# Optimization experiments

Hardware: AMD Instinct MI355X
Metric: run time of the kernel (lower is better)

## Reference

```python
import jax, jax.numpy as jnp
import numpy as np

B, L, D, K = 64, 1024, 128, 256
SQRT_2D = float(np.sqrt(2 * D))


def _biamlp(x1, x2, Wi, bi, Wq, bq):
    # proj to 2*D, norm-weighted fusion, avg-pool(2)*2 (== pairwise sum), L2-normalize over dim 1
    f1 = x1 @ Wi + bi          # [B, L, 2D]
    f2 = x2 @ Wq + bq          # [B, L, 2D]
    n1 = jnp.linalg.norm(f1)   # global L2 norm (scalar), as torch.norm(., p=2)
    n2 = jnp.linalg.norm(f2)
    e = (n1 / (n1 + n2)) * f1 + (n2 / (n1 + n2)) * f2
    b, l, c = e.shape
    z = e.reshape(b, l, c // 2, 2).mean(-1) * 2.0   # AvgPool1d(2,2) * 2 -> [B, L, D]
    denom = jnp.maximum(jnp.linalg.norm(z, axis=1, keepdims=True), 1e-12)  # F.normalize dim=1
    return z / denom


def _branch(feats, G_src, W_aff, W_c, W_lin, W_h):
    # feats: [B, L, D]; G_src: [B, L, 2D] (tensor fed to the affine projection)
    # a_j = affine(G_src^T): [B, 2D, L] @ [L, L]
    a_j = jnp.einsum('blc,lm->bcm', G_src, W_aff)            # [B, 2D, L]
    att = jnp.einsum('bld,bcl->bdc', feats, a_j) / SQRT_2D    # [B, D, 2D]
    C = jnp.tanh(att)
    H = jax.nn.relu(C @ W_c + jnp.einsum('bld,lk->bdk', feats, W_lin))  # [B, D, K]
    out = jnp.swapaxes(H @ W_h, 1, 2) + feats                 # [B, L, D]
    return out


def setup_inputs() -> dict:
    key = jax.random.key(0)
    ks = jax.random.split(key, 22)
    s = 0.02
    inp = {
        'f1_norm': jax.random.normal(ks[0], (B, L, D), jnp.float32),
        'f2_norm': jax.random.normal(ks[1], (B, L, D), jnp.float32),
        'f3_norm': jax.random.normal(ks[2], (B, L, D), jnp.float32),
        # BiAMLP params (feat_size = 128)
        'Wi': jax.random.normal(ks[3], (D, 2 * D), jnp.float32) * s,
        'bi': jax.random.normal(ks[4], (2 * D,), jnp.float32) * s,
        'Wq': jax.random.normal(ks[5], (D, 2 * D), jnp.float32) * s,
        'bq': jax.random.normal(ks[6], (2 * D,), jnp.float32) * s,
        # affine_{a,v,l}: Linear(l, l, bias=False), stored [in, out]
        'Wa_aff': jax.random.normal(ks[7], (L, L), jnp.float32) * s,
        'Wv_aff': jax.random.normal(ks[8], (L, L), jnp.float32) * s,
        'Wl_aff': jax.random.normal(ks[9], (L, L), jnp.float32) * s,
        # W_{a,v,t}: Linear(l, k)
        'W_a': jax.random.normal(ks[10], (L, K), jnp.float32) * s,
        'W_v': jax.random.normal(ks[11], (L, K), jnp.float32) * s,
        'W_t': jax.random.normal(ks[12], (L, K), jnp.float32) * s,
        # W_c{a,v,t}: Linear(2d, k)
        'W_ca': jax.random.normal(ks[13], (2 * D, K), jnp.float32) * s,
        'W_cv': jax.random.normal(ks[14], (2 * D, K), jnp.float32) * s,
        'W_ct': jax.random.normal(ks[15], (2 * D, K), jnp.float32) * s,
        # W_h{a,v,t}: Linear(k, l)
        'W_ha': jax.random.normal(ks[16], (K, L), jnp.float32) * s,
        'W_hv': jax.random.normal(ks[17], (K, L), jnp.float32) * s,
        'W_ht': jax.random.normal(ks[18], (K, L), jnp.float32) * s,
    }
    return inp


def reference(f1_norm, f2_norm, f3_norm, Wi, bi, Wq, bq, Wa_aff, Wv_aff, Wl_aff,
              W_a, W_v, W_t, W_ca, W_cv, W_ct, W_ha, W_hv, W_ht):
    txt, aud, vis = f1_norm, f2_norm, f3_norm
    # G2 = mode(txt, vis) and G3 = mode(aud, vis) are computed but unused in the
    # original (dead code); only G = G1 affects the output.
    G = _biamlp(txt, aud, Wi, bi, Wq, bq)        # [B, L, D]
    G_ag = jnp.concatenate([aud, G], axis=2)     # [B, L, 2D]
    G_lg = jnp.concatenate([txt, G], axis=2)     # [B, L, 2D]
    # NOTE: original bug preserved -- the visual branch projects G_ag (not G_vg).
    aud_out = _branch(aud, G_ag, Wa_aff, W_ca, W_a, W_ha)
    vis_out = _branch(vis, G_ag, Wv_aff, W_cv, W_v, W_hv)
    txt_out = _branch(txt, G_lg, Wl_aff, W_ct, W_t, W_ht)
    return (txt_out, aud_out, vis_out)
```

## Files before the change

kernel.cpp:

```cpp
#include <hip/hip_runtime.h>
#include <math.h>

typedef __attribute__((ext_vector_type(8))) short bf16x8;
typedef __attribute__((ext_vector_type(4))) float f32x4;

static constexpr int B_ = 64, L_ = 1024, D_ = 128, K_ = 256;
static constexpr long BLD_ = (long)B_ * L_ * D_;
static constexpr long LD_  = (long)L_ * D_;

__device__ __forceinline__ unsigned short f2b(float f) {
    unsigned int u = __builtin_bit_cast(unsigned int, f);
    u = (u + 0x7fffu + ((u >> 16) & 1u)) >> 16;
    return (unsigned short)u;
}
__device__ __forceinline__ float b2f(unsigned short h) {
    unsigned int u = ((unsigned int)h) << 16;
    return __builtin_bit_cast(float, u);
}

__device__ __forceinline__ void gl16(const unsigned short* g, unsigned short* s) {
    __builtin_amdgcn_global_load_lds(
        (const __attribute__((address_space(1))) unsigned int*)g,
        (__attribute__((address_space(3))) unsigned int*)s, 16, 0, 0);
}

struct TrEnt { const float* src; unsigned short* dst; int R, C, tr, start; };
struct TrTab { TrEnt e[17]; };

__device__ __forceinline__ void tr_body(const TrEnt& e, int tile, int t,
                                        unsigned short (*T)[72])
{
    int ntR = e.R >> 6, ntC = e.C >> 6;
    int nt = ntR * ntC;
    int bb = tile / nt, tt = tile - bb * nt;
    int ri = tt % ntR, ci = tt / ntR;
    const float* src = e.src + (long)bb * e.R * e.C + (long)(ri * 64) * e.C + ci * 64;
    if (!e.tr) {
        unsigned short* dstd = e.dst + (long)bb * e.R * e.C + (long)(ri * 64) * e.C + ci * 64;
        int r = t >> 2, cq = t & 3;
        const float* s = src + (long)r * e.C + cq * 16;
        unsigned short tmp[16];
        #pragma unroll
        for (int f = 0; f < 4; ++f) {
            float4 v = *(const float4*)(s + f * 4);
            tmp[f*4+0]=f2b(v.x); tmp[f*4+1]=f2b(v.y); tmp[f*4+2]=f2b(v.z); tmp[f*4+3]=f2b(v.w);
        }
        unsigned short* dp = dstd + (long)r * e.C + cq * 16;
        *(uint4*)&dp[0] = *(uint4*)&tmp[0];
        *(uint4*)&dp[8] = *(uint4*)&tmp[8];
        return;
    }
    unsigned short* dst = e.dst + (long)bb * e.R * e.C + (long)(ci * 64) * e.R + ri * 64;
    {
        int r = t >> 2, cq = t & 3;
        const float* s = src + (long)r * e.C + cq * 16;
        unsigned short tmp[16];
        #pragma unroll
        for (int f = 0; f < 4; ++f) {
            float4 v = *(const float4*)(s + f * 4);
            tmp[f*4+0]=f2b(v.x); tmp[f*4+1]=f2b(v.y); tmp[f*4+2]=f2b(v.z); tmp[f*4+3]=f2b(v.w);
        }
        *(uint4*)&T[r][cq*16]   = *(uint4*)&tmp[0];
        *(uint4*)&T[r][cq*16+8] = *(uint4*)&tmp[8];
    }
    __syncthreads();
    {
        int cr = t >> 2, rq = t & 3;
        unsigned short tmp[16];
        #pragma unroll
        for (int j = 0; j < 16; ++j) tmp[j] = T[rq*16 + j][cr];
        unsigned short* dp = dst + (long)cr * e.R + rq * 16;
        *(uint4*)&dp[0] = *(uint4*)&tmp[0];
        *(uint4*)&dp[8] = *(uint4*)&tmp[8];
    }
}

__global__ __launch_bounds__(256)
void trk(TrTab tab)
{
    __shared__ unsigned short T[64][72];
    int bid = blockIdx.x;
    int ei = 0;
    #pragma unroll
    for (int i = 1; i < 17; ++i) if (bid >= tab.e[i].start) ei = i;
    TrEnt e = tab.e[ei];
    tr_body(e, bid - e.start, threadIdx.x, T);
}

struct OpDesc {
    const unsigned short* A;
    long aOff0, aOff1, aOff2, sA;
    int lda;
    const unsigned short* B0;
    long bOff0, bOff1, bOff2, sB0;
    const unsigned short* B1;
    long sB1;
    int ldb;
    void* C;
    long sC;
    int ldc;
    const float* E0; const float* E1; const float* E2;
    float* ss;
    int Kd;
};

template<int EPI, int AF32, int TM>
__device__ __forceinline__ void gbody(const OpDesc& d, int bx, int by, int zrem,
                                      unsigned short (*As)[TM][32],
                                      unsigned short (*Bs)[128][32])
{
    const int tid = threadIdx.x;
    const long m0 = (long)bx * TM;
    const int n0 = by * 128;
    const int br = zrem >> 6, bb = zrem & 63;

    long aO = (br == 0 ? d.aOff0 : br == 1 ? d.aOff1 : d.aOff2) + (long)bb * d.sA;
    const unsigned short* A_ = d.A + aO;
    const float* Af = (const float*)d.A;
    const unsigned short* Bp;
    int nB = n0;
    if (d.B1 && n0 >= 128) { Bp = d.B1 + (long)bb * d.sB1; nB = n0 - 128; }
    else { Bp = d.B0 + (br == 0 ? d.bOff0 : br == 1 ? d.bOff1 : d.bOff2) + (long)bb * d.sB0; }

    const int w = tid >> 6, l = tid & 63;
    const int wm = (TM == 128) ? (w >> 1) : 0;
    const int wn = (TM == 128) ? (w & 1) : w;
    const int NJ = (TM == 128) ? 4 : 2;
    const int WS = (TM == 128) ? 64 : 32;
    const int fr = l & 15, kg = l >> 4;

    f32x4 acc[4][4];
    #pragma unroll
    for (int i = 0; i < 4; ++i)
        #pragma unroll
        for (int j = 0; j < 4; ++j)
            acc[i][j] = (f32x4){0.f, 0.f, 0.f, 0.f};

    const int sc8 = ((l & 3) ^ ((l >> 3) & 3)) * 8;
    const int rc  = (kg ^ ((fr >> 1) & 3)) * 8;

    auto stage = [&](int buf, int k0) {
        if (AF32) {
            int row = tid >> 1, half = tid & 1;
            const float* s = Af + (long)(m0 + row) * d.lda + k0 + half * 16;
            unsigned short tmp[16];
            #pragma unroll
            for (int f = 0; f < 4; ++f) {
                float4 v = *(const float4*)(s + f * 4);
                tmp[f*4+0]=f2b(v.x); tmp[f*4+1]=f2b(v.y); tmp[f*4+2]=f2b(v.z); tmp[f*4+3]=f2b(v.w);
            }
            int sw = (row >> 1) & 3;
            *(uint4*)&As[buf][row][((2*half    ) ^ sw) * 8] = *(uint4*)&tmp[0];
            *(uint4*)&As[buf][row][((2*half + 1) ^ sw) * 8] = *(uint4*)&tmp[8];
        } else if (TM == 128) {
            const unsigned short* ga = A_ + (m0 + 32*w + (l >> 2)) * (long)d.lda + k0 + sc8;
            gl16(ga,                    &As[buf][32*w][0]);
            gl16(ga + 16*(long)d.lda,   &As[buf][32*w + 16][0]);
        } else {
            const unsigned short* ga = A_ + (m0 + 16*w + (l >> 2)) * (long)d.lda + k0 + sc8;
            gl16(ga, &As[buf][16*w][0]);
        }
        const unsigned short* gb = Bp + (long)(nB + 32*w + (l >> 2)) * d.ldb + k0 + sc8;
        gl16(gb,                  &Bs[buf][32*w][0]);
        gl16(gb + 16*(long)d.ldb, &Bs[buf][32*w + 16][0]);
    };

    auto compute = [&](int cb) {
        bf16x8 af[4], bf[4];
        #pragma unroll
        for (int i = 0; i < 4; ++i) af[i] = *(const bf16x8*)&As[cb][wm*64 + i*16 + fr][rc];
        #pragma unroll
        for (int j = 0; j < NJ; ++j) bf[j] = *(const bf16x8*)&Bs[cb][wn*WS + j*16 + fr][rc];
        #pragma unroll
        for (int i = 0; i < 4; ++i)
            #pragma unroll
            for (int j = 0; j < NJ; ++j)
                acc[i][j] = __builtin_amdgcn_mfma_f32_16x16x32_bf16(af[i], bf[j], acc[i][j], 0, 0, 0);
    };

    const int nt = d.Kd >> 5;
    stage(0, 0);
    __syncthreads();
    for (int t = 0; t < nt; ++t) {
        if (t + 1 < nt) stage((t + 1) & 1, (t + 1) << 5);
        compute(t & 1);
        __syncthreads();
    }

    if (EPI == 4) {
        unsigned short* C = (unsigned short*)d.C;
        float lss = 0.f;
        #pragma unroll
        for (int i = 0; i < 4; ++i)
            #pragma unroll
            for (int j = 0; j < 4; ++j) {
                int cg = n0 + wn*64 + j*16 + fr;
                float bias = d.E0[cg];
                #pragma unroll
                for (int r = 0; r < 4; ++r) {
                    float v = acc[i][j][r] + bias;
                    lss += v * v;
                }
            }
        #pragma unroll
        for (int o = 32; o; o >>= 1) lss += __shfl_xor(lss, o);
        __shared__ float red4[4];
        if (l == 0) red4[w] = lss;
        float* eb = (float*)As;
        #pragma unroll
        for (int cc = 0; cc < 4; ++cc) {
            __syncthreads();
            #pragma unroll
            for (int j = 0; j < 4; ++j) {
                int cg = n0 + wn*64 + j*16 + fr;
                float bias = d.E0[cg];
                #pragma unroll
                for (int r = 0; r < 4; ++r)
                    eb[(wm*16 + kg*4 + r)*128 + wn*64 + j*16 + fr] = acc[cc][j][r] + bias;
            }
            __syncthreads();
            int lr = tid >> 3, pc = tid & 7;
            long gr = m0 + (lr < 16 ? cc*16 + lr : 48 + cc*16 + lr);
            unsigned short pk[8];
            #pragma unroll
            for (int e = 0; e < 8; ++e) {
                float v0 = eb[lr*128 + pc*16 + 2*e];
                float v1 = eb[lr*128 + pc*16 + 2*e + 1];
                pk[e] = f2b(v0 + v1);
            }
            *(uint4*)&C[gr * (long)d.ldc + (n0 >> 1) + pc*8] = *(uint4*)&pk[0];
        }
        if (tid == 0)
            d.ss[bx * 2 + by] = red4[0] + red4[1] + red4[2] + red4[3];
    } else if (TM == 64) {
        float* eb = (float*)As;
        #pragma unroll
        for (int cc = 0; cc < 4; ++cc) {
            __syncthreads();
            #pragma unroll
            for (int j = 0; j < 2; ++j)
                #pragma unroll
                for (int r = 0; r < 4; ++r)
                    eb[(kg*4 + r)*128 + wn*32 + j*16 + fr] = acc[cc][j][r];
            __syncthreads();
            unsigned short* C = (unsigned short*)d.C + (long)zrem * d.sC;
            int colx = (tid & 15) * 8;
            int lr = tid >> 4;
            long gr = m0 + cc*16 + lr;
            long gi = gr * (long)d.ldc + n0 + colx;
            unsigned short ov[8];
            if (EPI == 2) *(uint4*)ov = *(const uint4*)&C[gi];
            unsigned short pk[8];
            #pragma unroll
            for (int e = 0; e < 8; ++e) {
                float v = eb[lr*128 + colx + e];
                if (EPI == 1) v = tanhf(v * 0.0625f);
                if (EPI == 2) v = fmaxf(v + b2f(ov[e]), 0.f);
                pk[e] = f2b(v);
            }
            *(uint4*)&C[gi] = *(uint4*)&pk[0];
        }
    } else {
        float* eb = (float*)As;
        #pragma unroll
        for (int cc = 0; cc < 4; ++cc) {
            __syncthreads();
            #pragma unroll
            for (int j = 0; j < 4; ++j)
                #pragma unroll
                for (int r = 0; r < 4; ++r)
                    eb[(wm*16 + kg*4 + r)*128 + wn*64 + j*16 + fr] = acc[cc][j][r];
            __syncthreads();
            if (EPI == 3) {
                long off = (br == 2) ? 0L : (long)(br + 1) * BLD_;
                float* Co = (float*)d.C + off + (long)bb * LD_;
                const float* Ep = (br == 0 ? d.E0 : br == 1 ? d.E1 : d.E2) + (long)bb * LD_;
                int colx = (tid & 31) * 4;
                #pragma unroll
                for (int p = 0; p < 4; ++p) {
                    int lr = (tid >> 5) + 8 * p;
                    long gr = m0 + (lr < 16 ? cc*16 + lr : 48 + cc*16 + lr);
                    long gi = gr * (long)d.ldc + n0 + colx;
                    float4 v = *(float4*)&eb[lr*128 + colx];
                    float4 e4 = *(const float4*)&Ep[gi];
                    v.x += e4.x; v.y += e4.y; v.z += e4.z; v.w += e4.w;
                    *(float4*)&Co[gi] = v;
                }
            } else {
                unsigned short* C = (unsigned short*)d.C + (long)zrem * d.sC;
                int colx = (tid & 15) * 8;
                #pragma unroll
                for (int p = 0; p < 2; ++p) {
                    int lr = (tid >> 4) + 16 * p;
                    long gr = m0 + (lr < 16 ? cc*16 + lr : 48 + cc*16 + lr);
                    long gi = gr * (long)d.ldc + n0 + colx;
                    unsigned short ov[8];
                    if (EPI == 2) *(uint4*)ov = *(const uint4*)&C[gi];
                    unsigned short pk[8];
                    #pragma unroll
                    for (int e = 0; e < 8; ++e) {
                        float v = eb[lr*128 + colx + e];
                        if (EPI == 1) v = tanhf(v * 0.0625f);
                        if (EPI == 2) v = fmaxf(v + b2f(ov[e]), 0.f);
                        pk[e] = f2b(v);
                    }
                    *(uint4*)&C[gi] = *(uint4*)&pk[0];
                }
            }
        }
    }
}

template<int EPI0, int EPI1, int AF32, int SWZ, int TM>
__global__ __launch_bounds__(256)
void mg(OpDesc d0, OpDesc d1, int zsplit)
{
    __shared__ __align__(16) unsigned short As[2][TM][32];
    __shared__ __align__(16) unsigned short Bs[2][128][32];
    int bx, by, bz;
    if (SWZ) {
        int nwg = gridDim.x * gridDim.y * gridDim.z;
        int c = blockIdx.x + gridDim.x * (blockIdx.y + gridDim.y * blockIdx.z);
        int lid = (c & 7) * (nwg >> 3) + (c >> 3);
        bx = lid % gridDim.x; lid /= gridDim.x;
        by = lid % gridDim.y; bz = lid / gridDim.y;
    } else {
        bx = blockIdx.x; by = blockIdx.y; bz = blockIdx.z;
    }
    if (bz < zsplit) gbody<EPI0, AF32, TM>(d0, bx, by, bz, As, Bs);
    else             gbody<EPI1, AF32, TM>(d1, bx, by, bz - zsplit, As, Bs);
}

template<int EPI0, int EPI1, int SWZ, int TM>
__global__ __launch_bounds__(256)
void mgy(OpDesc d0, OpDesc d1, int ysplit)
{
    __shared__ __align__(16) unsigned short As[2][TM][32];
    __shared__ __align__(16) unsigned short Bs[2][128][32];
    int bx, by, bz;
    if (SWZ) {
        int nwg = gridDim.x * gridDim.y * gridDim.z;
        int c = blockIdx.x + gridDim.x * (blockIdx.y + gridDim.y * blockIdx.z);
        int lid = (c & 7) * (nwg >> 3) + (c >> 3);
        bx = lid % gridDim.x; lid /= gridDim.x;
        by = lid % gridDim.y; bz = lid / gridDim.y;
    } else {
        bx = blockIdx.x; by = blockIdx.y; bz = blockIdx.z;
    }
    if (by < ysplit) gbody<EPI0, 0, TM>(d0, bx, by, bz, As, Bs);
    else             gbody<EPI1, 0, TM>(d1, bx, by - ysplit, bz, As, Bs);
}

__global__ __launch_bounds__(256)
void mgbi(TrEnt e0, TrEnt e1, TrEnt e2, OpDesc dTxt, OpDesc dAud)
{
    __shared__ __align__(16) unsigned short As[2][128][32];
    __shared__ __align__(16) unsigned short Bs[2][128][32];
    int bid = blockIdx.x;
    if (bid < 6144) {
        TrEnt e = (bid < 2048) ? e0 : (bid < 4096) ? e1 : e2;
        tr_body(e, bid & 2047, threadIdx.x, (unsigned short (*)[72])As);
    } else {
        int rem = bid - 6144;
        int z = rem >> 10;
        int t = rem & 1023;
        gbody<4, 1, 128>(z ? dAud : dTxt, t >> 1, t & 1, 0, As, Bs);
    }
}

__global__ __launch_bounds__(256)
void k2z(unsigned short* __restrict__ q1, const unsigned short* __restrict__ q2,
         const float* __restrict__ partial, float* __restrict__ colssP)
{
    int t = threadIdx.x;
    float a = partial[t] + partial[t + 256] + partial[t + 512] + partial[t + 768];
    float bsum = partial[1024 + t] + partial[1280 + t] + partial[1536 + t] + partial[1792 + t];
    #pragma unroll
    for (int o = 32; o; o >>= 1) { a += __shfl_xor(a, o); bsum += __shfl_xor(bsum, o); }
    __shared__ float ra[4], rb[4];
    int wv = t >> 6;
    if ((t & 63) == 0) { ra[wv] = a; rb[wv] = bsum; }
    __syncthreads();
    float n1 = sqrtf(ra[0] + ra[1] + ra[2] + ra[3]);
    float n2 = sqrtf(rb[0] + rb[1] + rb[2] + rb[3]);
    float al = n1 / (n1 + n2), be = n2 / (n1 + n2);

    int b = blockIdx.x, lc = blockIdx.y;
    int d = t & 127, ls = t >> 7;
    long base = ((long)b * L_ + (long)lc * 64) * D_;
    float acc = 0.f;
    for (int ll = ls; ll < 64; ll += 2) {
        long idx = base + (long)ll * D_ + d;
        float zv = al * b2f(q1[idx]) + be * b2f(q2[idx]);
        q1[idx] = f2b(zv);
        acc += zv * zv;
    }
    __shared__ float red[256];
    red[t] = acc;
    __syncthreads();
    if (t < 128)
        colssP[((long)b * 16 + lc) * 128 + d] = red[t] + red[t + 128];
}

__global__ __launch_bounds__(256)
void k3nT(const unsigned short* __restrict__ z, const float* __restrict__ colssP,
          unsigned short* __restrict__ GT)
{
    __shared__ unsigned short T[128][136];
    int b = blockIdx.x, lt = blockIdx.y;
    int t = threadIdx.x;
    {
        int r = t >> 1, half = t & 1;
        const unsigned short* src = z + ((long)b * L_ + lt * 128 + r) * D_ + half * 64;
        #pragma unroll
        for (int q = 0; q < 8; ++q)
            *(uint4*)&T[r][half*64 + q*8] = *(const uint4*)(src + q*8);
    }
    __syncthreads();
    {
        int d = t >> 1, lh = t & 1;
        float s = 0.f;
        #pragma unroll
        for (int lc = 0; lc < 16; ++lc)
            s += colssP[((long)b * 16 + lc) * 128 + d];
        float inv = 1.f / fmaxf(sqrtf(s), 1e-12f);
        unsigned short tmp[64];
        #pragma unroll
        for (int j = 0; j < 64; ++j) tmp[j] = f2b(b2f(T[lh*64 + j][d]) * inv);
        unsigned short* dp = GT + ((long)b * D_ + d) * L_ + lt * 128 + lh * 64;
        #pragma unroll
        for (int q = 0; q < 8; ++q) *(uint4*)&dp[q*8] = *(uint4*)&tmp[q*8];
    }
}

extern "C" void kernel_launch(void* const* d_in, const int* in_sizes, int n_in,
                              void* d_out, int out_size, void* d_ws, size_t ws_size,
                              hipStream_t stream)
{
    const float* txt = (const float*)d_in[0];
    const float* aud = (const float*)d_in[1];
    const float* vis = (const float*)d_in[2];
    const float* Wi  = (const float*)d_in[3];
    const float* bi  = (const float*)d_in[4];
    const float* Wq  = (const float*)d_in[5];
    const float* bq  = (const float*)d_in[6];
    const float* Waff[3] = { (const float*)d_in[7], (const float*)d_in[8], (const float*)d_in[9] };
    const float* Wlin[3] = { (const float*)d_in[10], (const float*)d_in[11], (const float*)d_in[12] };
    const float* Wc[3]   = { (const float*)d_in[13], (const float*)d_in[14], (const float*)d_in[15] };
    const float* Wh[3]   = { (const float*)d_in[16], (const float*)d_in[17], (const float*)d_in[18] };

    unsigned short* w16 = (unsigned short*)d_ws;
    unsigned short* featT = w16;
    unsigned short* q1b   = featT + 3 * BLD_;
    unsigned short* q2b   = q1b + BLD_;
    unsigned short* WAb   = q2b + BLD_;
    unsigned short* WLTb  = WAb + 3145728;
    unsigned short* WCTb  = WLTb + 786432;
    unsigned short* WHTb  = WCTb + 196608;
    unsigned short* WiTb  = WHTb + 786432;
    unsigned short* WqTb  = WiTb + 32768;
    float* partial = (float*)(WqTb + 32768);
    float* colssP  = partial + 2048;
    unsigned short* Cm3 = q1b;
    unsigned short* Hb3 = q1b + 6291456;
    unsigned short* S2all = (unsigned short*)d_out;
    unsigned short* GT    = S2all + 3 * BLD_;

    TrTab tab;
    auto setE = [&](int i, const float* s, unsigned short* dst, int R, int C, int tr, int start) {
        tab.e[i].src = s; tab.e[i].dst = dst; tab.e[i].R = R; tab.e[i].C = C;
        tab.e[i].tr = tr; tab.e[i].start = start;
    };
    int st = 0;
    setE(0, Wi, WiTb, 128, 256, 1, st); st += 8;
    setE(1, Wq, WqTb, 128, 256, 1, st); st += 8;
    for (int i = 0; i < 3; ++i) { setE(2 + i, Wlin[i], WLTb + (long)i * 262144, 1024, 256, 1, st); st += 64; }
    for (int i = 0; i < 3; ++i) { setE(5 + i, Wc[i],   WCTb + (long)i * 65536,  256, 256, 1, st); st += 16; }
    for (int i = 0; i < 3; ++i) { setE(8 + i, Wh[i],   WHTb + (long)i * 262144, 256, 1024, 1, st); st += 64; }
    for (int i = 0; i < 3; ++i) { setE(11 + i, Waff[i], WAb + (long)i * 1048576, 1024, 1024, 0, st); st += 256; }
    for (int i = 14; i < 17; ++i) { tab.e[i].start = 1 << 30; tab.e[i].src = nullptr; }
    trk<<<st, 256, 0, stream>>>(tab);

    TrEnt eA = { aud, featT + 0,        1024, 128, 1, 0 };
    TrEnt eV = { vis, featT + BLD_,     1024, 128, 1, 0 };
    TrEnt eT = { txt, featT + 2 * BLD_, 1024, 128, 1, 0 };
    OpDesc dTxt = {}, dAud = {};
    dTxt.A = (const unsigned short*)txt; dTxt.lda = 128;
    dTxt.B0 = WiTb; dTxt.ldb = 128;
    dTxt.C = q1b; dTxt.ldc = 128;
    dTxt.E0 = bi; dTxt.ss = partial; dTxt.Kd = 128;
    dAud = dTxt;
    dAud.A = (const unsigned short*)aud; dAud.B0 = WqTb; dAud.C = q2b;
    dAud.E0 = bq; dAud.ss = partial + 1024;
    mgbi<<<8192, 256, 0, stream>>>(eA, eV, eT, dTxt, dAud);

    k2z<<<dim3(64, 16), 256, 0, stream>>>(q1b, q2b, partial, colssP);
    k3nT<<<dim3(64, 8), 256, 0, stream>>>(q1b, colssP, GT);

    OpDesc dS2 = {};
    dS2.A = featT; dS2.aOff0 = 0; dS2.aOff1 = BLD_; dS2.aOff2 = 2 * BLD_;
    dS2.sA = LD_; dS2.lda = 1024;
    dS2.B0 = WAb; dS2.bOff0 = 0; dS2.bOff1 = 1048576; dS2.bOff2 = 2097152;
    dS2.sB0 = 0; dS2.ldb = 1024;
    dS2.C = S2all; dS2.sC = LD_; dS2.ldc = 1024; dS2.Kd = 1024;
    OpDesc dU = {};
    dU.A = featT; dU.aOff0 = 0; dU.aOff1 = BLD_; dU.aOff2 = 2 * BLD_;
    dU.sA = LD_; dU.lda = 1024;
    dU.B0 = WLTb; dU.bOff0 = 0; dU.bOff1 = 262144; dU.bOff2 = 524288;
    dU.sB0 = 0; dU.ldb = 1024;
    dU.C = Hb3; dU.sC = 32768; dU.ldc = 256; dU.Kd = 1024;
    mgy<0, 0, 1, 128><<<dim3(1, 10, 192), 256, 0, stream>>>(dS2, dU, 8);

    OpDesc dAtt = {};
    dAtt.A = S2all; dAtt.aOff0 = 0; dAtt.aOff1 = 64 * LD_; dAtt.aOff2 = 128 * LD_;
    dAtt.sA = LD_; dAtt.lda = 1024;
    dAtt.B0 = featT; dAtt.bOff0 = 0; dAtt.bOff1 = 0; dAtt.bOff2 = 2 * BLD_;
    dAtt.sB0 = LD_;
    dAtt.B1 = GT; dAtt.sB1 = LD_; dAtt.ldb = 1024;
    dAtt.C = Cm3; dAtt.sC = 32768; dAtt.ldc = 256; dAtt.Kd = 1024;
    mg<1, 1, 0, 1, 64><<<dim3(2, 2, 192), 256, 0, stream>>>(dAtt, dAtt, 192);

    OpDesc dT = {};
    dT.A = Cm3; dT.aOff0 = 0; dT.aOff1 = 2097152; dT.aOff2 = 4194304;
    dT.sA = 32768; dT.lda = 256;
    dT.B0 = WCTb; dT.bOff0 = 0; dT.bOff1 = 65536; dT.bOff2 = 131072;
    dT.sB0 = 0; dT.ldb = 256;
    dT.C = Hb3; dT.sC = 32768; dT.ldc = 256; dT.Kd = 256;
    mg<2, 2, 0, 1, 64><<<dim3(2, 2, 192), 256, 0, stream>>>(dT, dT, 192);

    OpDesc dOut = {};
    dOut.A = WHTb; dOut.aOff0 = 0; dOut.aOff1 = 262144; dOut.aOff2 = 524288;
    dOut.sA = 0; dOut.lda = 256;
    dOut.B0 = Hb3; dOut.bOff0 = 0; dOut.bOff1 = 2097152; dOut.bOff2 = 4194304;
    dOut.sB0 = 32768; dOut.ldb = 256;
    dOut.C = d_out; dOut.ldc = 128;
    dOut.E0 = aud; dOut.E1 = vis; dOut.E2 = txt; dOut.Kd = 256;
    mg<3, 3, 0, 1, 128><<<dim3(8, 1, 192), 256, 0, stream>>>(dOut, dOut, 192);
}
```

Measured before the change: 286.7 us.

## Merge weight conversion into the feature-transpose launch and fold k2z into the projection GEMM

The large weight transposes and conversions (affine, lin, c, h) move out of the standalone trk launch and into the mgbi launch through a table lookup. Only the small Wi/Wq conversions, which the BiAMLP GEMM needs first, stay in a separate trk launch. The k2z fusion step now runs as extra blocks inside the S2/U GEMM launch (mgyk), and k3nT runs after that GEMM. This cuts launch count and lets the small elementwise work overlap GEMM tiles, at the cost of a per-block table scan and k2z blocks sharing the grid with GEMM blocks.

```diff
diff --git a/kernel.cpp b/kernel.cpp
--- a/kernel.cpp
+++ b/kernel.cpp
@@ -311,6 +311,40 @@
     }
 }
 
+__device__ __forceinline__ void k2z_body(unsigned short* q1, const unsigned short* q2,
+                                         const float* partial, float* colssP,
+                                         int b, int lc, float* sred)
+{
+    int t = threadIdx.x;
+    float a = partial[t] + partial[t + 256] + partial[t + 512] + partial[t + 768];
+    float bsum = partial[1024 + t] + partial[1280 + t] + partial[1536 + t] + partial[1792 + t];
+    #pragma unroll
+    for (int o = 32; o; o >>= 1) { a += __shfl_xor(a, o); bsum += __shfl_xor(bsum, o); }
+    float* ra = sred + 256;
+    float* rb = sred + 260;
+    int wv = t >> 6;
+    if ((t & 63) == 0) { ra[wv] = a; rb[wv] = bsum; }
+    __syncthreads();
+    float n1 = sqrtf(ra[0] + ra[1] + ra[2] + ra[3]);
+    float n2 = sqrtf(rb[0] + rb[1] + rb[2] + rb[3]);
+    float al = n1 / (n1 + n2), be = n2 / (n1 + n2);
+
+    int d = t & 127, ls = t >> 7;
+    long base = ((long)b * L_ + (long)lc * 64) * D_;
+    float acc = 0.f;
+    for (int ll = ls; ll < 64; ll += 2) {
+        long idx = base + (long)ll * D_ + d;
+        float zv = al * b2f(q1[idx]) + be * b2f(q2[idx]);
+        q1[idx] = f2b(zv);
+        acc += zv * zv;
+    }
+    __syncthreads();
+    sred[t] = acc;
+    __syncthreads();
+    if (t < 128)
+        colssP[((long)b * 16 + lc) * 128 + d] = sred[t] + sred[t + 128];
+}
+
 template<int EPI0, int EPI1, int AF32, int SWZ, int TM>
 __global__ __launch_bounds__(256)
 void mg(OpDesc d0, OpDesc d1, int zsplit)
@@ -331,75 +365,43 @@
     else             gbody<EPI1, AF32, TM>(d1, bx, by, bz - zsplit, As, Bs);
 }
 
-template<int EPI0, int EPI1, int SWZ, int TM>
 __global__ __launch_bounds__(256)
-void mgy(OpDesc d0, OpDesc d1, int ysplit)
-{
-    __shared__ __align__(16) unsigned short As[2][TM][32];
-    __shared__ __align__(16) unsigned short Bs[2][128][32];
-    int bx, by, bz;
-    if (SWZ) {
-        int nwg = gridDim.x * gridDim.y * gridDim.z;
-        int c = blockIdx.x + gridDim.x * (blockIdx.y + gridDim.y * blockIdx.z);
-        int lid = (c & 7) * (nwg >> 3) + (c >> 3);
-        bx = lid % gridDim.x; lid /= gridDim.x;
-        by = lid % gridDim.y; bz = lid / gridDim.y;
-    } else {
-        bx = blockIdx.x; by = blockIdx.y; bz = blockIdx.z;
-    }
-    if (by < ysplit) gbody<EPI0, 0, TM>(d0, bx, by, bz, As, Bs);
-    else             gbody<EPI1, 0, TM>(d1, bx, by - ysplit, bz, As, Bs);
-}
-
-__global__ __launch_bounds__(256)
-void mgbi(TrEnt e0, TrEnt e1, TrEnt e2, OpDesc dTxt, OpDesc dAud)
+void mgyk(OpDesc dS2, OpDesc dU,
+          unsigned short* q1, const unsigned short* q2,
+          const float* partial, float* colssP)
 {
     __shared__ __align__(16) unsigned short As[2][128][32];
     __shared__ __align__(16) unsigned short Bs[2][128][32];
     int bid = blockIdx.x;
-    if (bid < 6144) {
-        TrEnt e = (bid < 2048) ? e0 : (bid < 4096) ? e1 : e2;
-        tr_body(e, bid & 2047, threadIdx.x, (unsigned short (*)[72])As);
+    if (bid < 1024) {
+        k2z_body(q1, q2, partial, colssP, bid >> 4, bid & 15, (float*)As);
     } else {
-        int rem = bid - 6144;
+        int id = bid - 1024;
+        int lid = (id & 7) * 240 + (id >> 3);
+        int by = lid % 10, bz = lid / 10;
+        if (by < 8) gbody<0, 0, 128>(dS2, 0, by, bz, As, Bs);
+        else        gbody<0, 0, 128>(dU, 0, by - 8, bz, As, Bs);
+    }
+}
+
+__global__ __launch_bounds__(256)
+void mgbi(TrTab tab, OpDesc dTxt, OpDesc dAud)
+{
+    __shared__ __align__(16) unsigned short As[2][128][32];
+    __shared__ __align__(16) unsigned short Bs[2][128][32];
+    int bid = blockIdx.x;
+    if (bid < 7344) {
+        int ei = 0;
+        #pragma unroll
+        for (int i = 1; i < 17; ++i) if (bid >= tab.e[i].start) ei = i;
+        TrEnt e = tab.e[ei];
+        tr_body(e, bid - e.start, threadIdx.x, (unsigned short (*)[72])As);
+    } else {
+        int rem = bid - 7344;
         int z = rem >> 10;
         int t = rem & 1023;
         gbody<4, 1, 128>(z ? dAud : dTxt, t >> 1, t & 1, 0, As, Bs);
     }
-}
-
-__global__ __launch_bounds__(256)
-void k2z(unsigned short* __restrict__ q1, const unsigned short* __restrict__ q2,
-         const float* __restrict__ partial, float* __restrict__ colssP)
-{
-    int t = threadIdx.x;
-    float a = partial[t] + partial[t + 256] + partial[t + 512] + partial[t + 768];
-    float bsum = partial[1024 + t] + partial[1280 + t] + partial[1536 + t] + partial[1792 + t];
-    #pragma unroll
-    for (int o = 32; o; o >>= 1) { a += __shfl_xor(a, o); bsum += __shfl_xor(bsum, o); }
-    __shared__ float ra[4], rb[4];
-    int wv = t >> 6;
-    if ((t & 63) == 0) { ra[wv] = a; rb[wv] = bsum; }
-    __syncthreads();
-    float n1 = sqrtf(ra[0] + ra[1] + ra[2] + ra[3]);
-    float n2 = sqrtf(rb[0] + rb[1] + rb[2] + rb[3]);
-    float al = n1 / (n1 + n2), be = n2 / (n1 + n2);
-
-    int b = blockIdx.x, lc = blockIdx.y;
-    int d = t & 127, ls = t >> 7;
-    long base = ((long)b * L_ + (long)lc * 64) * D_;
-    float acc = 0.f;
-    for (int ll = ls; ll < 64; ll += 2) {
-        long idx = base + (long)ll * D_ + d;
-        float zv = al * b2f(q1[idx]) + be * b2f(q2[idx]);
-        q1[idx] = f2b(zv);
-        acc += zv * zv;
-    }
-    __shared__ float red[256];
-    red[t] = acc;
-    __syncthreads();
-    if (t < 128)
-        colssP[((long)b * 16 + lc) * 128 + d] = red[t] + red[t + 128];
 }
 
 __global__ __launch_bounds__(256)
@@ -466,24 +468,27 @@
     unsigned short* S2all = (unsigned short*)d_out;
     unsigned short* GT    = S2all + 3 * BLD_;
 
+    TrTab tw;
+    for (int i = 0; i < 17; ++i) { tw.e[i].start = 1 << 30; tw.e[i].src = nullptr; }
+    tw.e[0] = { Wi, WiTb, 128, 256, 1, 0 };
+    tw.e[1] = { Wq, WqTb, 128, 256, 1, 8 };
+    trk<<<16, 256, 0, stream>>>(tw);
+
     TrTab tab;
-    auto setE = [&](int i, const float* s, unsigned short* dst, int R, int C, int tr, int start) {
-        tab.e[i].src = s; tab.e[i].dst = dst; tab.e[i].R = R; tab.e[i].C = C;
-        tab.e[i].tr = tr; tab.e[i].start = start;
-    };
-    int st = 0;
-    setE(0, Wi, WiTb, 128, 256, 1, st); st += 8;
-    setE(1, Wq, WqTb, 128, 256, 1, st); st += 8;
-    for (int i = 0; i < 3; ++i) { setE(2 + i, Wlin[i], WLTb + (long)i * 262144, 1024, 256, 1, st); st += 64; }
-    for (int i = 0; i < 3; ++i) { setE(5 + i, Wc[i],   WCTb + (long)i * 65536,  256, 256, 1, st); st += 16; }
-    for (int i = 0; i < 3; ++i) { setE(8 + i, Wh[i],   WHTb + (long)i * 262144, 256, 1024, 1, st); st += 64; }
-    for (int i = 0; i < 3; ++i) { setE(11 + i, Waff[i], WAb + (long)i * 1048576, 1024, 1024, 0, st); st += 256; }
-    for (int i = 14; i < 17; ++i) { tab.e[i].start = 1 << 30; tab.e[i].src = nullptr; }
-    trk<<<st, 256, 0, stream>>>(tab);
-
-    TrEnt eA = { aud, featT + 0,        1024, 128, 1, 0 };
-    TrEnt eV = { vis, featT + BLD_,     1024, 128, 1, 0 };
-    TrEnt eT = { txt, featT + 2 * BLD_, 1024, 128, 1, 0 };
+    tab.e[0] = { aud, featT + 0,        1024, 128, 1, 0 };
+    tab.e[1] = { vis, featT + BLD_,     1024, 128, 1, 2048 };
+    tab.e[2] = { txt, featT + 2 * BLD_, 1024, 128, 1, 4096 };
+    for (int i = 0; i < 3; ++i)
+        tab.e[3 + i] = { Waff[i], WAb + (long)i * 1048576, 1024, 1024, 0, 6144 + i * 256 };
+    for (int i = 0; i < 3; ++i)
+        tab.e[6 + i] = { Wlin[i], WLTb + (long)i * 262144, 1024, 256, 1, 6912 + i * 64 };
+    for (int i = 0; i < 3; ++i)
+        tab.e[9 + i] = { Wc[i], WCTb + (long)i * 65536, 256, 256, 1, 7104 + i * 16 };
+    for (int i = 0; i < 3; ++i)
+        tab.e[12 + i] = { Wh[i], WHTb + (long)i * 262144, 256, 1024, 1, 7152 + i * 64 };
+    tab.e[15].start = 1 << 30; tab.e[15].src = nullptr;
+    tab.e[16].start = 1 << 30; tab.e[16].src = nullptr;
+
     OpDesc dTxt = {}, dAud = {};
     dTxt.A = (const unsigned short*)txt; dTxt.lda = 128;
     dTxt.B0 = WiTb; dTxt.ldb = 128;
@@ -492,10 +497,7 @@
     dAud = dTxt;
     dAud.A = (const unsigned short*)aud; dAud.B0 = WqTb; dAud.C = q2b;
     dAud.E0 = bq; dAud.ss = partial + 1024;
-    mgbi<<<8192, 256, 0, stream>>>(eA, eV, eT, dTxt, dAud);
-
-    k2z<<<dim3(64, 16), 256, 0, stream>>>(q1b, q2b, partial, colssP);
-    k3nT<<<dim3(64, 8), 256, 0, stream>>>(q1b, colssP, GT);
+    mgbi<<<9392, 256, 0, stream>>>(tab, dTxt, dAud);
 
     OpDesc dS2 = {};
     dS2.A = featT; dS2.aOff0 = 0; dS2.aOff1 = BLD_; dS2.aOff2 = 2 * BLD_;
@@ -509,7 +511,9 @@
     dU.B0 = WLTb; dU.bOff0 = 0; dU.bOff1 = 262144; dU.bOff2 = 524288;
     dU.sB0 = 0; dU.ldb = 1024;
     dU.C = Hb3; dU.sC = 32768; dU.ldc = 256; dU.Kd = 1024;
-    mgy<0, 0, 1, 128><<<dim3(1, 10, 192), 256, 0, stream>>>(dS2, dU, 8);
+    mgyk<<<2944, 256, 0, stream>>>(dS2, dU, q1b, q2b, partial, colssP);
+
+    k3nT<<<dim3(64, 8), 256, 0, stream>>>(q1b, colssP, GT);
 
     OpDesc dAtt = {};
     dAtt.A = S2all; dAtt.aOff0 = 0; dAtt.aOff1 = 64 * LD_; dAtt.aOff2 = 128 * LD_;
```

After: 288.3 us. No clear change (+0.6%).
